# Kernel tuning notes

Measured on AMD Instinct MI355X. Metric: run time of the kernel, lower is better.

Reference implementation:

```python
import jax, jax.numpy as jnp
import numpy as np

B, T, D, H, QK, V, M = 2, 2048, 1024, 16, 64, 64, 1024
SOFTCAP = 50.0


def apply_rope(x, positions, max_wavelength=10000.0):
    # x: (B, T, H, d), positions: (T,)
    d = x.shape[-1]
    fraction = 2.0 * jnp.arange(d // 2, dtype=jnp.float32) / d
    timescale = max_wavelength ** fraction                      # (d/2,)
    sinusoid = positions.astype(jnp.float32)[:, None] / timescale  # (T, d/2)
    sin = jnp.sin(sinusoid)[:, None, :]  # (T, 1, d/2) broadcasts over heads
    cos = jnp.cos(sinusoid)[:, None, :]
    x1, x2 = jnp.split(x, 2, axis=-1)
    out = jnp.concatenate([x1 * cos - x2 * sin, x2 * cos + x1 * sin], axis=-1)
    return out.astype(x.dtype)


def rms_norm(x, scale, eps=1e-6):
    var = jnp.mean(jnp.square(x.astype(jnp.float32)), axis=-1, keepdims=True)
    normed = x * jax.lax.rsqrt(var + eps).astype(x.dtype)
    return normed * (1.0 + scale).astype(x.dtype)


def setup_inputs() -> dict:
    key = jax.random.key(0)
    ks = jax.random.split(key, 10)
    s = 0.02
    # key-padding mask: per-batch kv valid lengths (all rows have >=1536 valid keys)
    kv_lens = jnp.array([1536, 2048], dtype=jnp.int32)
    mask = (jnp.arange(T)[None, :] < kv_lens[:, None])  # (B, Tk)
    mask = jnp.broadcast_to(mask[:, None, None, :], (B, 1, T, T))
    return {
        "q": jax.random.normal(ks[0], (B, T, D), jnp.float32),
        "kv": jax.random.normal(ks[1], (B, T, D), jnp.float32),
        "mask": mask,
        "q_positions": jnp.arange(T, dtype=jnp.int32),
        "kv_positions": jnp.arange(T, dtype=jnp.int32),
        "wq": jax.random.normal(ks[2], (D, H * QK), jnp.float32) * s,
        "bq": jnp.zeros((H * QK,), jnp.float32),
        "wk": jax.random.normal(ks[3], (D, H * QK), jnp.float32) * s,
        "bk": jnp.zeros((H * QK,), jnp.float32),
        "wv": jax.random.normal(ks[4], (D, H * V), jnp.float32) * s,
        "bv": jnp.zeros((H * V,), jnp.float32),
        "q_scale": jnp.zeros((QK,), jnp.float32),
        "k_scale": jnp.zeros((QK,), jnp.float32),
        "wo": jax.random.normal(ks[5], (H * V, M), jnp.float32) * s,
        "bo": jnp.zeros((M,), jnp.float32),
    }


def reference(q, kv, mask, q_positions, kv_positions,
              wq, bq, wk, bk, wv, bv, q_scale, k_scale, wo, bo):
    qh = (q @ wq + bq).reshape(B, T, H, QK)
    kh = (kv @ wk + bk).reshape(B, T, H, QK)
    vh = (kv @ wv + bv).reshape(B, T, H, V)
    # QK RMSNorm
    qh = rms_norm(qh, q_scale)
    kh = rms_norm(kh, k_scale)
    # RoPE
    qh = apply_rope(qh, q_positions)
    kh = apply_rope(kh, kv_positions)
    # softcapped, masked attention
    logits = jnp.einsum("bthd,bThd->bhtT", qh, kh) / np.sqrt(QK).astype(jnp.float32)
    logits = SOFTCAP * jnp.tanh(logits / SOFTCAP)
    logits = jnp.where(mask, logits, -1e9)
    log_probs = jax.nn.log_softmax(logits, axis=-1)
    probs = jnp.exp(log_probs)
    probs = jnp.where(mask, probs, 0.0)
    # normalized attention entropy (B, H, T)
    entropy = -jnp.sum(probs * log_probs, axis=-1) / jnp.log(mask.sum(axis=-1))
    attn = jnp.einsum("bhtT,bThd->bthd", probs, vh).reshape(B, T, H * V)
    out = attn @ wo + bo
    return out, entropy
```

## Files before the change

### kernel.cpp

```cpp
#include <hip/hip_runtime.h>

#define BB 2
#define TT 2048
#define DD 1024
#define HH 16
#define QKD 64
#define VD 64
#define MD 1024

typedef _Float16 half4 __attribute__((ext_vector_type(4)));
typedef _Float16 half8 __attribute__((ext_vector_type(8)));
typedef __fp16 fp16x2 __attribute__((ext_vector_type(2)));
typedef float f32x4 __attribute__((ext_vector_type(4)));
typedef unsigned short us8 __attribute__((ext_vector_type(8)));
typedef unsigned short us4 __attribute__((ext_vector_type(4)));

__device__ __forceinline__ unsigned short f2h(float x){
    union { _Float16 h; unsigned short u; } c; c.h = (_Float16)x; return c.u;
}

__device__ __forceinline__ void gl16(const void* g, void* l){
    __builtin_amdgcn_global_load_lds(
        (const __attribute__((address_space(1))) void*)g,
        (__attribute__((address_space(3))) void*)l, 16, 0, 0);
}

__global__ __launch_bounds__(256) void k_prep(const float* __restrict__ q,
                                              const float* __restrict__ kv,
                                              unsigned short* __restrict__ q_bf,
                                              unsigned short* __restrict__ kv_bf,
                                              const float* __restrict__ w0,
                                              const float* __restrict__ w1,
                                              const float* __restrict__ w2,
                                              const float* __restrict__ w3,
                                              unsigned short* __restrict__ o0,
                                              unsigned short* __restrict__ o1,
                                              unsigned short* __restrict__ o2,
                                              unsigned short* __restrict__ o3,
                                              const int* __restrict__ qpos,
                                              const int* __restrict__ kpos,
                                              float* __restrict__ tabq,
                                              float* __restrict__ tabk,
                                              const unsigned char* __restrict__ mask,
                                              int* __restrict__ kvlen){
    __shared__ float smem[64*65];
    int bid = blockIdx.x, tid = threadIdx.x;
    if (bid < 8192){
        const int n = BB*TT*DD/4;
        int idx = bid*256 + tid;
        const float* src = (idx < n) ? q : kv;
        unsigned short* dst = (idx < n) ? q_bf : kv_bf;
        int i = ((idx < n) ? idx : idx - n)*4;
        const float4 v = *(const float4*)(src + i);
        us4 o; o.x = f2h(v.x); o.y = f2h(v.y); o.z = f2h(v.z); o.w = f2h(v.w);
        *(us4*)(dst + i) = o;
    } else if (bid < 9216){
        int idx2 = bid - 8192;
        int z = idx2 >> 8;
        int rc2 = idx2 & 255;
        const float* in = (z==0) ? w0 : (z==1) ? w1 : (z==2) ? w2 : w3;
        unsigned short* out = (z==0) ? o0 : (z==1) ? o1 : (z==2) ? o2 : o3;
        float (*ts)[65] = (float(*)[65])smem;
        int r0 = (rc2 & 15)*64, c0 = (rc2 >> 4)*64;
        int lr = tid >> 4, lc = (tid & 15)*4;
#pragma unroll
        for (int i = 0; i < 4; ++i){
            const float4 v = *(const float4*)(in + (long)(r0 + lr + i*16)*1024 + c0 + lc);
            ts[lr+i*16][lc+0] = v.x; ts[lr+i*16][lc+1] = v.y;
            ts[lr+i*16][lc+2] = v.z; ts[lr+i*16][lc+3] = v.w;
        }
        __syncthreads();
        int oc = tid >> 2, rc = (tid & 3)*16;
        int ocp = oc;
        if (z < 2){
            int blk = oc >> 4;
            ocp = (blk == 1) ? oc + 16 : ((blk == 2) ? oc - 16 : oc);
        }
        us8 o0v, o1v;
#pragma unroll
        for (int j = 0; j < 8; ++j){ o0v[j] = f2h(ts[rc+j][ocp]); o1v[j] = f2h(ts[rc+8+j][ocp]); }
        *(us8*)(out + (long)(c0+oc)*1024 + r0 + rc)     = o0v;
        *(us8*)(out + (long)(c0+oc)*1024 + r0 + rc + 8) = o1v;
    } else if (bid < 9728){
        int gi = (bid - 9216)*256 + tid;
        const int* pos = (gi < 65536) ? qpos : kpos;
        float* tab = (gi < 65536) ? tabq : tabk;
        int idx = gi & 65535;
        int t = idx >> 5, f = idx & 31;
        float invts = expf(-((float)f*(1.f/32.f)) * 9.210340371976184f);
        float ph = (float)pos[t]*invts;
        ((float2*)tab)[idx] = make_float2(sinf(ph), cosf(ph));
    } else {
        int* red = (int*)smem;
        int b = bid - 9728;
        bool bytemode = (mask[1] != 0);
        int cnt = 0;
        for (int j = tid; j < TT; j += 256){
            long e = (long)b*TT*TT + j;
            if (bytemode) cnt += (mask[e] != 0);
            else          cnt += (((const unsigned int*)mask)[e] != 0);
        }
        red[tid] = cnt; __syncthreads();
        for (int s = 128; s > 0; s >>= 1){ if (tid < s) red[tid] += red[tid+s]; __syncthreads(); }
        if (tid == 0) kvlen[b] = red[0];
    }
}

#define GEMM_CORE(A_, Bt_, abase, bbase)                                            \
    int srow = l >> 3;                                                              \
    int scol = ((l & 7) ^ srow)*8;                                                  \
    int swb = lg ^ (li & 7);                                                        \
    const unsigned short* ga[4]; const unsigned short* gb[2];                       \
    _Pragma("unroll")                                                               \
    for (int i = 0; i < 4; ++i) ga[i] = A_  + (long)(m0 + w*32 + i*8 + srow)*1024 + scol; \
    _Pragma("unroll")                                                               \
    for (int i = 0; i < 2; ++i) gb[i] = Bt_ + (long)(n0 + w*16 + i*8 + srow)*1024 + scol; \
    _Pragma("unroll")                                                               \
    for (int i = 0; i < 4; ++i) gl16(ga[i], abase + (w*32 + i*8)*128);              \
    _Pragma("unroll")                                                               \
    for (int i = 0; i < 2; ++i) gl16(gb[i], bbase + (w*16 + i*8)*128);              \
    __syncthreads();                                                                \
    for (int ks = 0; ks < 16; ++ks){                                                \
        int cur = ks & 1;                                                           \
        if (ks + 1 < 16){                                                           \
            char* an = abase + (cur^1)*16384;                                       \
            char* bn = bbase + (cur^1)*8192;                                        \
            _Pragma("unroll")                                                       \
            for (int i = 0; i < 4; ++i){ ga[i] += 64; gl16(ga[i], an + (w*32 + i*8)*128); } \
            _Pragma("unroll")                                                       \
            for (int i = 0; i < 2; ++i){ gb[i] += 64; gl16(gb[i], bn + (w*16 + i*8)*128); } \
        }                                                                           \
        const char* ac = abase + cur*16384;                                         \
        const char* bc = bbase + cur*8192;                                          \
        _Pragma("unroll")                                                           \
        for (int kk = 0; kk < 2; ++kk){                                             \
            int co = ((kk*4) ^ swb)*16;                                             \
            half8 af[4], bf[2];                                                     \
            _Pragma("unroll")                                                       \
            for (int mi = 0; mi < 4; ++mi) af[mi] = *(const half8*)(ac + (wm + mi*16 + li)*128 + co); \
            _Pragma("unroll")                                                       \
            for (int ni = 0; ni < 2; ++ni) bf[ni] = *(const half8*)(bc + (wn + ni*16 + li)*128 + co); \
            _Pragma("unroll")                                                       \
            for (int mi = 0; mi < 4; ++mi)                                          \
                _Pragma("unroll")                                                   \
                for (int ni = 0; ni < 2; ++ni)                                      \
                    acc[mi][ni] = __builtin_amdgcn_mfma_f32_16x16x32_f16(af[mi], bf[ni], acc[mi][ni], 0, 0, 0); \
        }                                                                           \
        __syncthreads();                                                            \
    }

__global__ __launch_bounds__(256) void k_gemm3(const unsigned short* __restrict__ q_bf,
                                               const unsigned short* __restrict__ kv_bf,
                                               const unsigned short* __restrict__ wqt,
                                               const unsigned short* __restrict__ wkt,
                                               const unsigned short* __restrict__ wvt,
                                               const float* __restrict__ bq,
                                               const float* __restrict__ bk,
                                               const float* __restrict__ bv,
                                               const float* __restrict__ qscale,
                                               const float* __restrict__ kscale,
                                               const float* __restrict__ tabq,
                                               const float* __restrict__ tabk,
                                               unsigned short* __restrict__ Qr,
                                               unsigned short* __restrict__ Kr,
                                               unsigned short* __restrict__ VTb){
    __shared__ float4 smem_[3072];
    char* abase = (char*)smem_;
    char* bbase = abase + 32768;
    int flat = blockIdx.x;
    int virt = (flat & 7)*192 + (flat >> 3);
    int z = virt >> 9;
    int rem = virt & 511;
    int m0 = (rem >> 4)*128;
    int nx = rem & 15;
    int n0 = nx*64;
    const unsigned short* A  = (z == 0) ? q_bf : kv_bf;
    const unsigned short* Bt = (z == 0) ? wqt : (z == 1) ? wkt : wvt;

    int tid = threadIdx.x, l = tid & 63, w = tid >> 6;
    int lg = l >> 4, li = l & 15;
    int wm = (w >> 1)*64, wn = (w & 1)*32;
    f32x4 zero = {0.f,0.f,0.f,0.f};
    f32x4 acc[4][2];
#pragma unroll
    for (int mi = 0; mi < 4; ++mi){ acc[mi][0] = zero; acc[mi][1] = zero; }
    GEMM_CORE(A, Bt, abase, bbase)

    int hd = nx;
    if (z < 2){
        const float* bias  = (z == 0) ? bq : bk;
        const float* scale = (z == 0) ? qscale : kscale;
        const float* tab   = (z == 0) ? tabq : tabk;
        unsigned short* out = (z == 0) ? Qr : Kr;
        float* hs = (float*)smem_;
        int d0 = (wn >> 1) + li;
        float b0 = bias[hd*64 + d0];
        float b1 = bias[hd*64 + d0 + 32];
        float ssp[4][4];
#pragma unroll
        for (int mi = 0; mi < 4; ++mi)
#pragma unroll
            for (int r = 0; r < 4; ++r){
                float x0 = acc[mi][0][r] + b0;
                float x1 = acc[mi][1][r] + b1;
                ssp[mi][r] = x0*x0 + x1*x1;
            }
#pragma unroll
        for (int m = 1; m < 16; m <<= 1)
#pragma unroll
            for (int mi = 0; mi < 4; ++mi)
#pragma unroll
                for (int r = 0; r < 4; ++r) ssp[mi][r] += __shfl_xor(ssp[mi][r], m);
        if (li == 0){
#pragma unroll
            for (int mi = 0; mi < 4; ++mi)
#pragma unroll
                for (int r = 0; r < 4; ++r)
                    hs[(wm + mi*16 + lg*4 + r)*2 + (w & 1)] = ssp[mi][r];
        }
        __syncthreads();
        float sc0 = 1.f + scale[d0];
        float sc1 = 1.f + scale[d0 + 32];
#pragma unroll
        for (int mi = 0; mi < 4; ++mi)
#pragma unroll
            for (int r = 0; r < 4; ++r){
                int row = wm + mi*16 + lg*4 + r;
                float ss = hs[row*2] + hs[row*2 + 1];
                float rstd = rsqrtf(ss*(1.f/64.f) + 1e-6f);
                float x0 = (acc[mi][0][r] + b0)*rstd*sc0;
                float x1 = (acc[mi][1][r] + b1)*rstd*sc1;
                int gm = m0 + row;
                int bb = gm >> 11, t = gm & 2047;
                float2 scv = ((const float2*)tab)[t*32 + d0];
                float o0 = x0*scv.y - x1*scv.x;
                float o1 = x1*scv.y + x0*scv.x;
                long obase = ((long)(bb*HH + hd)*TT + t)*64;
                out[obase + d0]      = f2h(o0);
                out[obase + d0 + 32] = f2h(o1);
            }
    } else {
        float* Tt = (float*)smem_;
#pragma unroll
        for (int mi = 0; mi < 4; ++mi)
#pragma unroll
            for (int ni = 0; ni < 2; ++ni){
                int col = wn + ni*16 + li;
                float bb = bv[hd*64 + col];
#pragma unroll
                for (int r = 0; r < 4; ++r)
                    Tt[col*133 + wm + mi*16 + lg*4 + r] = acc[mi][ni][r] + bb;
            }
        __syncthreads();
        int bb2 = m0 >> 11, t0 = m0 & 2047;
        int vd = tid >> 2, sg = (tid & 3)*32;
        long ob = ((long)(bb2*HH + hd)*64 + vd)*TT + t0 + sg;
#pragma unroll
        for (int c = 0; c < 4; ++c){
            us8 o;
#pragma unroll
            for (int j = 0; j < 8; ++j) o[j] = f2h(Tt[vd*133 + sg + c*8 + j]);
            *(us8*)(VTb + ob + c*8) = o;
        }
    }
}

__global__ __launch_bounds__(256) void k_gemm(const unsigned short* __restrict__ A,
                                              const unsigned short* __restrict__ Bt,
                                              const float* __restrict__ bias,
                                              float* __restrict__ C, int N){
    __shared__ float4 smem_[3072];
    char* abase = (char*)smem_;
    char* bbase = abase + 32768;
    int flat = blockIdx.x;
    int virt = (flat & 7)*64 + (flat >> 3);
    int m0 = (virt >> 4)*128, n0 = (virt & 15)*64;
    int tid = threadIdx.x, l = tid & 63, w = tid >> 6;
    int lg = l >> 4, li = l & 15;
    int wm = (w >> 1)*64, wn = (w & 1)*32;
    f32x4 zero = {0.f,0.f,0.f,0.f};
    f32x4 acc[4][2];
#pragma unroll
    for (int mi = 0; mi < 4; ++mi){ acc[mi][0] = zero; acc[mi][1] = zero; }
    GEMM_CORE(A, Bt, abase, bbase)
#pragma unroll
    for (int mi = 0; mi < 4; ++mi){
#pragma unroll
        for (int ni = 0; ni < 2; ++ni){
            int row = m0 + wm + mi*16 + lg*4;
            int col = n0 + wn + ni*16 + li;
            float bb = bias[col];
#pragma unroll
            for (int r = 0; r < 4; ++r)
                C[(long)(row + r)*N + col] = acc[mi][ni][r] + bb;
        }
    }
}

__global__ __launch_bounds__(512) void k_attn(const unsigned short* __restrict__ Qr,
                                              const unsigned short* __restrict__ Kr,
                                              const unsigned short* __restrict__ VT,
                                              const int* __restrict__ kvlen,
                                              unsigned short* __restrict__ attnb,
                                              float* __restrict__ ent){
    __shared__ unsigned short Ks[2][64][64];
    __shared__ unsigned short Vs[2][64][64];
    int tid = threadIdx.x;
    int l = tid & 63, w = tid >> 6;
    int lg = l >> 4, li = l & 15;
    int flat = blockIdx.x;
    int xcd = flat & 7;
    int idx = flat >> 3;
    int qt = idx & 15;
    int g = idx >> 4;
    int bh = xcd*2 + (g & 1) + (g >> 1)*16;
    int b = bh >> 4, h = bh & 15;
    long qk0 = (long)bh * TT * 64;
    long vt0 = (long)bh * 64 * TT;
    int kvl = kvlen[b];
    int q0 = qt*128 + w*16;

    half8 qf[2];
#pragma unroll
    for (int kk = 0; kk < 2; ++kk)
        qf[kk] = *(const half8*)(Qr + qk0 + (long)(q0 + li)*64 + kk*32 + lg*8);

    int srow = l >> 3;
    int scol = ((l & 7) ^ srow)*8;
    const unsigned short* gK = Kr + qk0 + (long)(w*8 + srow)*64 + scol;
    const unsigned short* gV = VT + vt0 + (long)(w*8 + srow)*TT + scol;
    char* ksb = (char*)Ks;
    char* vsb = (char*)Vs;
    int swb = (lg >> 1) ^ (li & 7);
    int off8 = (lg & 1)*8;

    gl16(gK, ksb + w*8*128);
    gl16(gV, vsb + w*8*128);
    __syncthreads();

    f32x4 zero = {0.f,0.f,0.f,0.f};
    f32x4 oacc[4];
#pragma unroll
    for (int jv = 0; jv < 4; ++jv) oacc[jv] = zero;
    float l4[4]  = {0.f,0.f,0.f,0.f};
    float s14[4] = {0.f,0.f,0.f,0.f};

    const float PA = 0.18033688f;
    const float PB = -3.7570183e-7f;

    int nkv = (kvl + 63) >> 6;
    for (int kt = 0; kt < nkv; ++kt){
        int cur = kt & 1;
        const char* kc = ksb + cur*8192;
        const char* vc = vsb + cur*8192;
        if (kt + 1 < nkv){
            gK += 4096;
            gV += 64;
            gl16(gK, ksb + (cur^1)*8192 + w*8*128);
            gl16(gV, vsb + (cur^1)*8192 + w*8*128);
        }
        f32x4 sacc[4];
#pragma unroll
        for (int jt = 0; jt < 4; ++jt) sacc[jt] = zero;
#pragma unroll
        for (int kk = 0; kk < 2; ++kk){
            int co = ((kk*4 + lg) ^ (li & 7))*16;
#pragma unroll
            for (int jt = 0; jt < 4; ++jt){
                half8 kf = *(const half8*)(kc + (jt*16 + li)*128 + co);
                sacc[jt] = __builtin_amdgcn_mfma_f32_16x16x32_f16(kf, qf[kk], sacc[jt], 0, 0, 0);
            }
        }
        float xs2[4][4];
        bool tail = (kt*64 + 64 > kvl);
        if (tail){
#pragma unroll
            for (int jt = 0; jt < 4; ++jt){
#pragma unroll
                for (int r = 0; r < 4; ++r){
                    float u = sacc[jt][r];
                    float v = u*(PA + u*u*PB);
                    xs2[jt][r] = (kt*64 + jt*16 + lg*4 + r < kvl) ? v : -1e30f;
                }
            }
        } else {
#pragma unroll
            for (int jt = 0; jt < 4; ++jt){
#pragma unroll
                for (int r = 0; r < 4; ++r){
                    float u = sacc[jt][r];
                    xs2[jt][r] = u*(PA + u*u*PB);
                }
            }
        }
        float p[4][4];
#pragma unroll
        for (int jt = 0; jt < 4; ++jt){
#pragma unroll
            for (int r = 0; r < 4; ++r){
                float pp = exp2f(xs2[jt][r]);
                p[jt][r] = pp;
                l4[r]  += pp;
                s14[r] += pp * xs2[jt][r];
            }
        }
        half4 pa[4];
#pragma unroll
        for (int kk = 0; kk < 4; ++kk){
            union { half4 v; fp16x2 h2[2]; } up;
            up.h2[0] = __builtin_amdgcn_cvt_pkrtz(p[kk][0], p[kk][1]);
            up.h2[1] = __builtin_amdgcn_cvt_pkrtz(p[kk][2], p[kk][3]);
            pa[kk] = up.v;
        }
#pragma unroll
        for (int kk = 0; kk < 4; ++kk){
            int co = (((kk*2) ^ swb))*16 + off8;
#pragma unroll
            for (int jv = 0; jv < 4; ++jv){
                half4 vf = *(const half4*)(vc + (jv*16 + li)*128 + co);
                oacc[jv] = __builtin_amdgcn_mfma_f32_16x16x16f16(pa[kk], vf, oacc[jv], 0, 0, 0);
            }
        }
        __syncthreads();
    }

    float l_r  = (l4[0] + l4[1]) + (l4[2] + l4[3]);
    float s1_r = (s14[0] + s14[1]) + (s14[2] + s14[3]);
    l_r  += __shfl_xor(l_r, 16);  l_r  += __shfl_xor(l_r, 32);
    s1_r += __shfl_xor(s1_r, 16); s1_r += __shfl_xor(s1_r, 32);

    float invl = 1.f / l_r;
    float invr[4];
#pragma unroll
    for (int r = 0; r < 4; ++r) invr[r] = __shfl(invl, lg*4 + r);
#pragma unroll
    for (int jv = 0; jv < 4; ++jv){
#pragma unroll
        for (int r = 0; r < 4; ++r){
            int qrow = q0 + lg*4 + r;
            attnb[((long)b*TT + qrow)*1024 + h*64 + jv*16 + li] = f2h(oacc[jv][r]*invr[r]);
        }
    }
    if (l < 16){
        const float LN2 = 0.6931471805599453f;
        float lse = logf(l_r);
        float s1n = s1_r*LN2;
        ent[(long)bh*TT + q0 + li] = (lse - s1n*invl) / logf((float)kvl);
    }
}

extern "C" void kernel_launch(void* const* d_in, const int* in_sizes, int n_in,
                              void* d_out, int out_size, void* d_ws, size_t ws_size,
                              hipStream_t stream){
    (void)in_sizes; (void)n_in; (void)out_size; (void)ws_size;
    const float* q      = (const float*)d_in[0];
    const float* kv     = (const float*)d_in[1];
    const unsigned char* mask = (const unsigned char*)d_in[2];
    const int*   qpos   = (const int*)d_in[3];
    const int*   kpos   = (const int*)d_in[4];
    const float* wq     = (const float*)d_in[5];
    const float* bq     = (const float*)d_in[6];
    const float* wk     = (const float*)d_in[7];
    const float* bk     = (const float*)d_in[8];
    const float* wv     = (const float*)d_in[9];
    const float* bv     = (const float*)d_in[10];
    const float* qscale = (const float*)d_in[11];
    const float* kscale = (const float*)d_in[12];
    const float* wo     = (const float*)d_in[13];
    const float* bo     = (const float*)d_in[14];
    float* out = (float*)d_out;
    float* ent = out + (long)BB*TT*MD;

    char* ws = (char*)d_ws;
    unsigned short* wqt   = (unsigned short*)(ws);
    unsigned short* wkt   = (unsigned short*)(ws + 2097152L);
    unsigned short* wvt   = (unsigned short*)(ws + 4194304L);
    unsigned short* wot   = (unsigned short*)(ws + 6291456L);
    unsigned short* q_bf  = (unsigned short*)(ws + 8388608L);
    unsigned short* kv_bf = (unsigned short*)(ws + 16777216L);
    unsigned short* Qr    = (unsigned short*)(ws + 25165824L);
    unsigned short* Kr    = (unsigned short*)(ws + 33554432L);
    unsigned short* VTb   = (unsigned short*)(ws + 41943040L);
    unsigned short* attnb = (unsigned short*)(ws + 50331648L);
    float*          tabq  = (float*)(ws + 58720256L);
    float*          tabk  = (float*)(ws + 59244544L);
    int*            kvln  = (int*)(ws + 59768832L);

    k_prep<<<9730, 256, 0, stream>>>(q, kv, q_bf, kv_bf,
                                     wq, wk, wv, wo, wqt, wkt, wvt, wot,
                                     qpos, kpos, tabq, tabk, mask, kvln);

    k_gemm3<<<1536, 256, 0, stream>>>(q_bf, kv_bf, wqt, wkt, wvt,
                                      bq, bk, bv, qscale, kscale,
                                      tabq, tabk, Qr, Kr, VTb);

    k_attn<<<512, 512, 0, stream>>>(Qr, Kr, VTb, kvln, attnb, ent);

    k_gemm<<<512, 256, 0, stream>>>(attnb, wot, bo, out, 1024);
}
```

Measured before the change: 142.4 us.

## Stage K/V tiles through registers instead of direct global-to-LDS loads

Replaces the asynchronous global_load_lds copies of the next K and V tiles with ordinary 16-byte global loads into registers. These are issued before the QK^T MFMAs and written into the swizzled LDS double buffer after the PV MFMAs, so the global latency is meant to hide behind compute. It also adds a third term to the tanh softcap polynomial, which is an accuracy change rather than a speed one. The four per-lane row-sum and entropy partial accumulators are merged into single scalars, which lengthens the add dependency chain. The register staging raises VGPR pressure and adds LDS store instructions in exchange for more control over when copies happen.

```diff
diff --git a/kernel.cpp b/kernel.cpp
--- a/kernel.cpp
+++ b/kernel.cpp
@@ -325,39 +325,43 @@
     for (int kk = 0; kk < 2; ++kk)
         qf[kk] = *(const half8*)(Qr + qk0 + (long)(q0 + li)*64 + kk*32 + lg*8);
 
-    int srow = l >> 3;
-    int scol = ((l & 7) ^ srow)*8;
-    const unsigned short* gK = Kr + qk0 + (long)(w*8 + srow)*64 + scol;
-    const unsigned short* gV = VT + vt0 + (long)(w*8 + srow)*TT + scol;
+    int r0s = tid >> 3;
+    int kcs = (tid & 7)*8;
+    int sws = (((tid & 7) ^ (r0s & 7)))*16;
     char* ksb = (char*)Ks;
     char* vsb = (char*)Vs;
     int swb = (lg >> 1) ^ (li & 7);
     int off8 = (lg & 1)*8;
 
-    gl16(gK, ksb + w*8*128);
-    gl16(gV, vsb + w*8*128);
+    {
+        us8 ka = *(const us8*)(Kr + qk0 + (long)r0s*64 + kcs);
+        us8 va = *(const us8*)(VT + vt0 + (long)r0s*TT + kcs);
+        *(us8*)(ksb + r0s*128 + sws) = ka;
+        *(us8*)(vsb + r0s*128 + sws) = va;
+    }
     __syncthreads();
 
     f32x4 zero = {0.f,0.f,0.f,0.f};
     f32x4 oacc[4];
 #pragma unroll
     for (int jv = 0; jv < 4; ++jv) oacc[jv] = zero;
-    float l4[4]  = {0.f,0.f,0.f,0.f};
-    float s14[4] = {0.f,0.f,0.f,0.f};
+    float l_r = 0.f, s1_r = 0.f;
 
     const float PA = 0.18033688f;
     const float PB = -3.7570183e-7f;
+    const float PC = 9.3925458e-13f;
 
     int nkv = (kvl + 63) >> 6;
     for (int kt = 0; kt < nkv; ++kt){
         int cur = kt & 1;
         const char* kc = ksb + cur*8192;
         const char* vc = vsb + cur*8192;
-        if (kt + 1 < nkv){
-            gK += 4096;
-            gV += 64;
-            gl16(gK, ksb + (cur^1)*8192 + w*8*128);
-            gl16(gV, vsb + (cur^1)*8192 + w*8*128);
+        us8 ka, va;
+        bool pref = (kt + 1 < nkv);
+        if (pref){
+            int k0n = (kt+1)*64;
+            ka = *(const us8*)(Kr + qk0 + (long)(k0n + r0s)*64 + kcs);
+            va = *(const us8*)(VT + vt0 + (long)r0s*TT + k0n + kcs);
         }
         f32x4 sacc[4];
 #pragma unroll
@@ -379,7 +383,8 @@
 #pragma unroll
                 for (int r = 0; r < 4; ++r){
                     float u = sacc[jt][r];
-                    float v = u*(PA + u*u*PB);
+                    float z2 = u*u;
+                    float v = u*(PA + z2*(PB + z2*PC));
                     xs2[jt][r] = (kt*64 + jt*16 + lg*4 + r < kvl) ? v : -1e30f;
                 }
             }
@@ -389,7 +394,8 @@
 #pragma unroll
                 for (int r = 0; r < 4; ++r){
                     float u = sacc[jt][r];
-                    xs2[jt][r] = u*(PA + u*u*PB);
+                    float z2 = u*u;
+                    xs2[jt][r] = u*(PA + z2*(PB + z2*PC));
                 }
             }
         }
@@ -400,8 +406,8 @@
             for (int r = 0; r < 4; ++r){
                 float pp = exp2f(xs2[jt][r]);
                 p[jt][r] = pp;
-                l4[r]  += pp;
-                s14[r] += pp * xs2[jt][r];
+                l_r  += pp;
+                s1_r += pp * xs2[jt][r];
             }
         }
         half4 pa[4];
@@ -421,11 +427,14 @@
                 oacc[jv] = __builtin_amdgcn_mfma_f32_16x16x16f16(pa[kk], vf, oacc[jv], 0, 0, 0);
             }
         }
+        if (pref){
+            int nb = (kt+1) & 1;
+            *(us8*)(ksb + nb*8192 + r0s*128 + sws) = ka;
+            *(us8*)(vsb + nb*8192 + r0s*128 + sws) = va;
+        }
         __syncthreads();
     }
 
-    float l_r  = (l4[0] + l4[1]) + (l4[2] + l4[3]);
-    float s1_r = (s14[0] + s14[1]) + (s14[2] + s14[3]);
     l_r  += __shfl_xor(l_r, 16);  l_r  += __shfl_xor(l_r, 32);
     s1_r += __shfl_xor(s1_r, 16); s1_r += __shfl_xor(s1_r, 32);
 
```

Result: faster. 137.7 us (-3.3%).
